# Kernel optimization log

Measured on AMD Instinct MI355X. Metric: run time of the kernel, lower is better.

## Reference

```python
import jax, jax.numpy as jnp
import numpy as np

B, Cin, Cout, H, W, K, S, P = 8, 128, 128, 64, 64, 3, 1, 1


def setup_inputs() -> dict:
    key = jax.random.key(0)
    k1, k2, k3 = jax.random.split(key, 3)
    x = jax.random.normal(k1, (B, Cin, H, W), jnp.float32)
    # offset-predicting conv weight (zero-init in the original; use small random for a nontrivial test)
    w_offset = jax.random.normal(k2, (2 * K * K, Cin, K, K), jnp.float32) * 0.01
    # deformable conv weight, uniform(-stdv, stdv) with stdv = 1/sqrt(Cin*K*K)
    stdv = 1.0 / np.sqrt(Cin * K * K)
    w = jax.random.uniform(k3, (Cout, Cin, K, K), jnp.float32, -stdv, stdv)
    return {"x": x, "w_offset": w_offset, "w": w}


def _conv2d(x, w, stride, pad):
    return jax.lax.conv_general_dilated(
        x, w, (stride, stride), [(pad, pad), (pad, pad)],
        dimension_numbers=("NCHW", "OIHW", "NCHW"))


def _deform_conv(x, offset, w, stride, pad):
    # x: [B,C,H,W]; offset: [B,2*K*K,Ho,Wo] as (dy,dx) pairs per kernel tap; w: [Cout,C,K,K]
    Bb, C, Hh, Ww = x.shape
    Co, _, Kk, _ = w.shape
    _, _, Ho, Wo = offset.shape
    KK = Kk * Kk
    off = offset.reshape(Bb, KK, 2, Ho, Wo)
    dy, dx = off[:, :, 0], off[:, :, 1]              # [B,KK,Ho,Wo]

    ky, kx = jnp.meshgrid(jnp.arange(Kk), jnp.arange(Kk), indexing="ij")
    ky = ky.reshape(KK).astype(x.dtype)
    kx = kx.reshape(KK).astype(x.dtype)
    oy = (jnp.arange(Ho) * stride - pad).astype(x.dtype)
    ox = (jnp.arange(Wo) * stride - pad).astype(x.dtype)

    # absolute sampling coordinates per kernel tap: [B,KK,Ho,Wo]
    py = oy[None, None, :, None] + ky[None, :, None, None] + dy
    px = ox[None, None, None, :] + kx[None, :, None, None] + dx

    y0 = jnp.floor(py)
    x0 = jnp.floor(px)
    ly = py - y0
    lx = px - x0
    y0i = y0.astype(jnp.int32)
    x0i = x0.astype(jnp.int32)

    xf = x.reshape(Bb, C, Hh * Ww)

    def gather(yi, xi):
        valid = (yi >= 0) & (yi < Hh) & (xi >= 0) & (xi < Ww)
        yc = jnp.clip(yi, 0, Hh - 1)
        xc = jnp.clip(xi, 0, Ww - 1)
        idx = (yc * Ww + xc).reshape(Bb, -1)          # [B, KK*Ho*Wo]
        v = jax.vmap(lambda xb, ib: xb[:, ib])(xf, idx)  # [B, C, KK*Ho*Wo]
        return v * valid.reshape(Bb, 1, -1).astype(x.dtype)

    v00 = gather(y0i, x0i)
    v01 = gather(y0i, x0i + 1)
    v10 = gather(y0i + 1, x0i)
    v11 = gather(y0i + 1, x0i + 1)

    wy = ly.reshape(Bb, 1, -1)
    wx = lx.reshape(Bb, 1, -1)
    sampled = (v00 * (1 - wy) * (1 - wx) + v01 * (1 - wy) * wx
               + v10 * wy * (1 - wx) + v11 * wy * wx)   # [B, C, KK*Ho*Wo]
    sampled = sampled.reshape(Bb, C, KK, Ho * Wo)

    out = jnp.einsum("bckl,ock->bol", sampled, w.reshape(Co, C, KK))
    return out.reshape(Bb, Co, Ho, Wo)


def reference(x, w_offset, w):
    offset = _conv2d(x, w_offset, S, P)   # [B, 2*K*K, Ho, Wo]
    return _deform_conv(x, offset, w, S, P)
```

## Files before the change

### kernel.cpp

```cpp
#include <hip/hip_runtime.h>
#include <hip/hip_bf16.h>
#include <math.h>


typedef _Float16 f16x8 __attribute__((ext_vector_type(8)));
typedef _Float16 h2    __attribute__((ext_vector_type(2)));
typedef float    f32x4 __attribute__((ext_vector_type(4)));

__global__ __launch_bounds__(256) void prep_weights(
    const float* __restrict__ w, const float* __restrict__ woff,
    _Float16* __restrict__ wT, _Float16* __restrict__ woffT) {
    int idx = blockIdx.x * 256 + threadIdx.x;
    if (idx < 147456) {
        int c  = idx & 127;
        int co = (idx >> 7) & 127;
        int kk = idx >> 14;
        wT[idx] = (_Float16)w[co * 1152 + c * 9 + kk];
    }
    if (idx < 36864) {
        int c  = idx & 127;
        int oc = (idx >> 7) & 31;
        int kk = idx >> 12;
        woffT[idx] = (oc < 18) ? (_Float16)woff[oc * 1152 + c * 9 + kk] : (_Float16)0.f;
    }
}

__global__ __launch_bounds__(256) void transpose_nchw_nhwc(
    const float* __restrict__ x, unsigned* __restrict__ xT) {
    __shared__ float tile[128][65];
    int bh = blockIdx.x;
    int b = bh >> 6, h = bh & 63;
    const float* src = x + b * 524288 + h * 64;
    for (int idx = threadIdx.x; idx < 8192; idx += 256) {
        int c = idx >> 6, ww = idx & 63;
        tile[c][ww] = src[c * 4096 + ww];
    }
    __syncthreads();
    unsigned* dst = xT + (size_t)bh * 4096;
    for (int idx = threadIdx.x; idx < 4096; idx += 256) {
        int ww = idx >> 6, c2 = (idx & 63) * 2;
        union { h2 h; unsigned u; } p;
        p.h = h2{(_Float16)tile[c2][ww], (_Float16)tile[c2 + 1][ww]};
        dst[idx] = p.u;
    }
}

__global__ __launch_bounds__(512, 4) void deform_fused(
    const _Float16* __restrict__ xT,
    const _Float16* __restrict__ wT,
    const _Float16* __restrict__ woffT,
    float* __restrict__ out) {
    __shared__ unsigned short s_tile[2][8192];
    __shared__ float  s_off[18][64];
    __shared__ int4   s_pix[576];
    __shared__ float4 s_wt[576];

    int raw = blockIdx.x;
    int b  = raw & 7;
    int ho = raw >> 3;
    int t = threadIdx.x, l = t & 63, w = t >> 6;
    int lr = l & 15, lg = l >> 4;
    const char* xb = (const char*)xT + (size_t)b * 1048576;

    {
        int m4 = w >> 1, n2 = w & 1;
        f16x8 A[2][4];
        f32x4 oacc = {0.f, 0.f, 0.f, 0.f};
        auto loadA = [&](int kk, f16x8* dst) {
            int y = ho + kk / 3 - 1;
            int xcol = m4 * 16 + lr + kk % 3 - 1;
            bool valid = ((unsigned)y < 64u) && ((unsigned)xcol < 64u);
            int yc = min(max(y, 0), 63), xc = min(max(xcol, 0), 63);
            const char* p = xb + ((yc * 64 + xc) * 128 + lg * 8) * 2;
            _Float16 m = (_Float16)(valid ? 1.f : 0.f);
#pragma unroll
            for (int kg = 0; kg < 4; ++kg)
                dst[kg] = *(const f16x8*)(p + kg * 64) * m;
        };
        loadA(0, A[0]);
#pragma unroll
        for (int kk = 0; kk < 9; ++kk) {
            if (kk < 8) loadA(kk + 1, A[(kk + 1) & 1]);
            const _Float16* wo = woffT + (kk * 32 + n2 * 16 + lr) * 128 + lg * 8;
#pragma unroll
            for (int kg = 0; kg < 4; ++kg)
                oacc = __builtin_amdgcn_mfma_f32_16x16x32_f16(
                    A[kk & 1][kg], *(const f16x8*)(wo + kg * 32), oacc, 0, 0, 0);
        }
        int oc = n2 * 16 + lr;
        if (oc < 18) {
#pragma unroll
            for (int r = 0; r < 4; ++r)
                s_off[oc][m4 * 16 + lg * 4 + r] = oacc[r];
        }
    }
    __syncthreads();

    for (int e = t; e < 576; e += 512) {
        int pos = e & 63, kk = e >> 6;
        float dy = s_off[2 * kk][pos], dx = s_off[2 * kk + 1][pos];
        float py = (float)(ho + kk / 3 - 1) + dy;
        float px = (float)(pos + kk % 3 - 1) + dx;
        float y0f = floorf(py), x0f = floorf(px);
        float ly = py - y0f, lx = px - x0f;
        int y0 = (int)y0f, x0 = (int)x0f;
        int y1 = y0 + 1, x1 = x0 + 1;
        float my0 = ((unsigned)y0 < 64u) ? 1.f : 0.f;
        float my1 = ((unsigned)y1 < 64u) ? 1.f : 0.f;
        float mx0 = ((unsigned)x0 < 64u) ? 1.f : 0.f;
        float mx1 = ((unsigned)x1 < 64u) ? 1.f : 0.f;
        int y0c = min(max(y0, 0), 63), y1c = min(max(y1, 0), 63);
        int x0c = min(max(x0, 0), 63), x1c = min(max(x1, 0), 63);
        s_pix[e] = make_int4((y0c * 64 + x0c) * 256, (y0c * 64 + x1c) * 256,
                             (y1c * 64 + x0c) * 256, (y1c * 64 + x1c) * 256);
        s_wt[e] = make_float4((1.f - ly) * (1.f - lx) * my0 * mx0,
                              (1.f - ly) * lx * my0 * mx1,
                              ly * (1.f - lx) * my1 * mx0,
                              ly * lx * my1 * mx1);
    }
    __syncthreads();

    int pg = t >> 5;
    int cq = t & 31;
    int cb = w * 16;
    int coff = cq * 8;
    f32x4 acc[4] = {{0.f,0.f,0.f,0.f},{0.f,0.f,0.f,0.f},{0.f,0.f,0.f,0.f},{0.f,0.f,0.f,0.f}};
    f16x8 W[2][4];
    uint2 u[4][4];

    auto issueW = [&](int kk, f16x8* Wd) {
        const _Float16* wr = wT + (kk * 128 + cb + lr) * 128 + lg * 8;
#pragma unroll
        for (int kg = 0; kg < 4; ++kg)
            Wd[kg] = *(const f16x8*)(wr + kg * 32);
    };
    auto issueG = [&](int kk) {
#pragma unroll
        for (int i = 0; i < 4; ++i) {
            int pos = pg + i * 16;
            int4 pix = s_pix[kk * 64 + pos];
            u[i][0] = *(const uint2*)(xb + pix.x + coff);
            u[i][1] = *(const uint2*)(xb + pix.y + coff);
            u[i][2] = *(const uint2*)(xb + pix.z + coff);
            u[i][3] = *(const uint2*)(xb + pix.w + coff);
        }
    };
    auto processW = [&](int kk, int buf) {
        char* tp = (char*)s_tile[buf];
#pragma unroll
        for (int i = 0; i < 4; ++i) {
            int pos = pg + i * 16;
            float4 wt = s_wt[kk * 64 + pos];
            h2 w0 = h2{(_Float16)wt.x, (_Float16)wt.x};
            h2 w1 = h2{(_Float16)wt.y, (_Float16)wt.y};
            h2 w2 = h2{(_Float16)wt.z, (_Float16)wt.z};
            h2 w3 = h2{(_Float16)wt.w, (_Float16)wt.w};
            union { uint2 u2; h2 h[2]; } a0, a1, a2, a3, r;
            a0.u2 = u[i][0]; a1.u2 = u[i][1]; a2.u2 = u[i][2]; a3.u2 = u[i][3];
            r.h[0] = w0 * a0.h[0] + w1 * a1.h[0] + w2 * a2.h[0] + w3 * a3.h[0];
            r.h[1] = w0 * a0.h[1] + w1 * a1.h[1] + w2 * a2.h[1] + w3 * a3.h[1];
            *(uint2*)(tp + pos * 256 + (((cq >> 1) ^ (pos & 7)) << 4) + (cq & 1) * 8) = r.u2;
        }
    };

    issueW(0, W[0]);
    issueG(0);
    processW(0, 0);
    __syncthreads();

#pragma unroll
    for (int kk = 0; kk < 9; ++kk) {
        if (kk < 8) {
            issueW(kk + 1, W[(kk + 1) & 1]);
            issueG(kk + 1);
        }
        __builtin_amdgcn_sched_barrier(0);
        {
            char* rp = (char*)s_tile[kk & 1];
#pragma unroll
            for (int kg = 0; kg < 4; ++kg) {
                int slot = kg * 4 + lg;
#pragma unroll
                for (int n = 0; n < 4; ++n) {
                    int row = n * 16 + lr;
                    f16x8 Bf = *(const f16x8*)(rp + row * 256 + ((slot ^ (row & 7)) << 4));
                    acc[n] = __builtin_amdgcn_mfma_f32_16x16x32_f16(W[kk & 1][kg], Bf, acc[n], 0, 0, 0);
                }
            }
        }
        __builtin_amdgcn_sched_barrier(0);
        if (kk < 8) processW(kk + 1, (kk + 1) & 1);
        __syncthreads();
    }

    float* ob = out + ((size_t)(b * 128 + cb + lg * 4)) * 4096 + ho * 64;
#pragma unroll
    for (int n = 0; n < 4; ++n) {
#pragma unroll
        for (int r = 0; r < 4; ++r)
            ob[r * 4096 + n * 16 + lr] = acc[n][r];
    }
}

extern "C" void kernel_launch(void* const* d_in, const int* in_sizes, int n_in,
                              void* d_out, int out_size, void* d_ws, size_t ws_size,
                              hipStream_t stream) {
    const float* x    = (const float*)d_in[0];
    const float* woff = (const float*)d_in[1];
    const float* w    = (const float*)d_in[2];
    float* out = (float*)d_out;

    _Float16* wT    = (_Float16*)d_ws;
    _Float16* woffT = (_Float16*)((char*)d_ws + 294912);
    _Float16* xT    = (_Float16*)((char*)d_ws + 368640);

    prep_weights<<<576, 256, 0, stream>>>(w, woff, wT, woffT);
    transpose_nchw_nhwc<<<512, 256, 0, stream>>>(x, (unsigned*)xT);
    deform_fused<<<512, 512, 0, stream>>>(xT, wT, woffT, out);
}
```

Before: 144.5 us.

## Split each output row across two blocks with half-width tiles and wider gathers

Each block now handles 32 output pixels of a row instead of 64, which doubles the grid to 1024 blocks and raises launch bounds to 8 waves per SIMD. Shared memory is roughly halved, and pixel indices are stored as ushort4. The gather now loads 16-byte chunks per thread, one pixel per 16 threads, instead of 8-byte chunks. The main weights are reloaded each tap without double buffering. The aim is higher occupancy and more latency hiding for the gather, at the cost of redundant offset-conv work: half the waves compute duplicate offsets, and every block reloads the full weight set.

```diff
diff --git a/kernel.cpp b/kernel.cpp
--- a/kernel.cpp
+++ b/kernel.cpp
@@ -45,62 +45,66 @@
     }
 }
 
-__global__ __launch_bounds__(512, 4) void deform_fused(
+__global__ __launch_bounds__(512, 8) void deform_fused(
     const _Float16* __restrict__ xT,
     const _Float16* __restrict__ wT,
     const _Float16* __restrict__ woffT,
     float* __restrict__ out) {
-    __shared__ unsigned short s_tile[2][8192];
-    __shared__ float  s_off[18][64];
-    __shared__ int4   s_pix[576];
-    __shared__ float4 s_wt[576];
+    __shared__ unsigned short s_tile[2][4096];
+    __shared__ ushort4 s_pix[288];
+    __shared__ float4  s_wt[288];
+    __shared__ float   s_off[18][32];
 
     int raw = blockIdx.x;
-    int b  = raw & 7;
-    int ho = raw >> 3;
+    int b    = raw & 7;
+    int rest = raw >> 3;
+    int ho   = rest >> 1;
+    int pos0 = (rest & 1) * 32;
     int t = threadIdx.x, l = t & 63, w = t >> 6;
     int lr = l & 15, lg = l >> 4;
     const char* xb = (const char*)xT + (size_t)b * 1048576;
 
     {
-        int m4 = w >> 1, n2 = w & 1;
-        f16x8 A[2][4];
+        int m = w & 1, n = (w >> 1) & 1, dup = w >> 2;
+        f16x8 A[2][4], Bc[4];
         f32x4 oacc = {0.f, 0.f, 0.f, 0.f};
         auto loadA = [&](int kk, f16x8* dst) {
-            int y = ho + kk / 3 - 1;
-            int xcol = m4 * 16 + lr + kk % 3 - 1;
-            bool valid = ((unsigned)y < 64u) && ((unsigned)xcol < 64u);
-            int yc = min(max(y, 0), 63), xc = min(max(xcol, 0), 63);
-            const char* p = xb + ((yc * 64 + xc) * 128 + lg * 8) * 2;
-            _Float16 m = (_Float16)(valid ? 1.f : 0.f);
+            int y  = ho + kk / 3 - 1;
+            int xc = pos0 + m * 16 + lr + kk % 3 - 1;
+            bool valid = ((unsigned)y < 64u) && ((unsigned)xc < 64u);
+            int yc = min(max(y, 0), 63), xcc = min(max(xc, 0), 63);
+            const char* p = xb + ((yc * 64 + xcc) << 8) + lg * 16;
+            _Float16 mk = (_Float16)(valid ? 1.f : 0.f);
 #pragma unroll
             for (int kg = 0; kg < 4; ++kg)
-                dst[kg] = *(const f16x8*)(p + kg * 64) * m;
+                dst[kg] = *(const f16x8*)(p + kg * 64) * mk;
         };
         loadA(0, A[0]);
 #pragma unroll
         for (int kk = 0; kk < 9; ++kk) {
+            const _Float16* wo = woffT + ((kk * 32 + n * 16 + lr) << 7) + lg * 8;
+#pragma unroll
+            for (int kg = 0; kg < 4; ++kg)
+                Bc[kg] = *(const f16x8*)(wo + kg * 32);
             if (kk < 8) loadA(kk + 1, A[(kk + 1) & 1]);
-            const _Float16* wo = woffT + (kk * 32 + n2 * 16 + lr) * 128 + lg * 8;
 #pragma unroll
             for (int kg = 0; kg < 4; ++kg)
-                oacc = __builtin_amdgcn_mfma_f32_16x16x32_f16(
-                    A[kk & 1][kg], *(const f16x8*)(wo + kg * 32), oacc, 0, 0, 0);
+                oacc = __builtin_amdgcn_mfma_f32_16x16x32_f16(A[kk & 1][kg], Bc[kg], oacc, 0, 0, 0);
         }
-        int oc = n2 * 16 + lr;
-        if (oc < 18) {
+        int oc = n * 16 + lr;
+        if (dup == 0 && oc < 18) {
 #pragma unroll
             for (int r = 0; r < 4; ++r)
-                s_off[oc][m4 * 16 + lg * 4 + r] = oacc[r];
+                s_off[oc][m * 16 + lg * 4 + r] = oacc[r];
         }
     }
     __syncthreads();
 
-    for (int e = t; e < 576; e += 512) {
-        int pos = e & 63, kk = e >> 6;
-        float dy = s_off[2 * kk][pos], dx = s_off[2 * kk + 1][pos];
+    if (t < 288) {
+        int p32 = t & 31, kk = t >> 5;
+        float dy = s_off[2 * kk][p32], dx = s_off[2 * kk + 1][p32];
         float py = (float)(ho + kk / 3 - 1) + dy;
-        float px = (float)(pos + kk % 3 - 1) + dx;
+        float px = (float)(pos0 + p32 + kk % 3 - 1) + dx;
         float y0f = floorf(py), x0f = floorf(px);
         float ly = py - y0f, lx = px - x0f;
         int y0 = (int)y0f, x0 = (int)x0f;
@@ -111,69 +115,59 @@
         float mx1 = ((unsigned)x1 < 64u) ? 1.f : 0.f;
         int y0c = min(max(y0, 0), 63), y1c = min(max(y1, 0), 63);
         int x0c = min(max(x0, 0), 63), x1c = min(max(x1, 0), 63);
-        s_pix[e] = make_int4((y0c * 64 + x0c) * 256, (y0c * 64 + x1c) * 256,
-                             (y1c * 64 + x0c) * 256, (y1c * 64 + x1c) * 256);
-        s_wt[e] = make_float4((1.f - ly) * (1.f - lx) * my0 * mx0,
+        s_pix[t] = make_ushort4((unsigned short)(y0c * 64 + x0c),
+                                (unsigned short)(y0c * 64 + x1c),
+                                (unsigned short)(y1c * 64 + x0c),
+                                (unsigned short)(y1c * 64 + x1c));
+        s_wt[t] = make_float4((1.f - ly) * (1.f - lx) * my0 * mx0,
                               (1.f - ly) * lx * my0 * mx1,
                               ly * (1.f - lx) * my1 * mx0,
                               ly * lx * my1 * mx1);
     }
     __syncthreads();
 
-    int pg = t >> 5;
-    int cq = t & 31;
-    int cb = w * 16;
-    int coff = cq * 8;
-    f32x4 acc[4] = {{0.f,0.f,0.f,0.f},{0.f,0.f,0.f,0.f},{0.f,0.f,0.f,0.f},{0.f,0.f,0.f,0.f}};
-    f16x8 W[2][4];
-    uint2 u[4][4];
-
-    auto issueW = [&](int kk, f16x8* Wd) {
-        const _Float16* wr = wT + (kk * 128 + cb + lr) * 128 + lg * 8;
+    int p32 = t >> 4;
+    int cq  = t & 15;
+    int cb  = w * 16;
+    f32x4 acc[2] = {{0.f,0.f,0.f,0.f},{0.f,0.f,0.f,0.f}};
+    uint4 u[4];
+
+    auto issueG = [&](int kk) {
+        ushort4 pc = s_pix[kk * 32 + p32];
+        const char* bb = xb + cq * 16;
+        u[0] = *(const uint4*)(bb + ((int)pc.x << 8));
+        u[1] = *(const uint4*)(bb + ((int)pc.y << 8));
+        u[2] = *(const uint4*)(bb + ((int)pc.z << 8));
+        u[3] = *(const uint4*)(bb + ((int)pc.w << 8));
+    };
+    auto blend = [&](int kk, int buf) {
+        float4 wt = s_wt[kk * 32 + p32];
+        h2 w0 = h2{(_Float16)wt.x, (_Float16)wt.x};
+        h2 w1 = h2{(_Float16)wt.y, (_Float16)wt.y};
+        h2 w2 = h2{(_Float16)wt.z, (_Float16)wt.z};
+        h2 w3 = h2{(_Float16)wt.w, (_Float16)wt.w};
+        union { uint4 q; h2 h[4]; } c0, c1, c2, c3, r;
+        c0.q = u[0]; c1.q = u[1]; c2.q = u[2]; c3.q = u[3];
+#pragma unroll
+        for (int j = 0; j < 4; ++j)
+            r.h[j] = w0 * c0.h[j] + w1 * c1.h[j] + w2 * c2.h[j] + w3 * c3.h[j];
+        char* tpb = (char*)s_tile[buf];
+        *(uint4*)(tpb + p32 * 256 + ((cq ^ (p32 & 15)) << 4)) = r.q;
+    };
+
+    issueG(0);
+    blend(0, 0);
+    __syncthreads();
+
+#pragma unroll
+    for (int kk = 0; kk < 9; ++kk) {
+        f16x8 Wf[4];
+        const _Float16* wr = wT + ((kk * 128 + cb + lr) << 7) + lg * 8;
 #pragma unroll
         for (int kg = 0; kg < 4; ++kg)
-            Wd[kg] = *(const f16x8*)(wr + kg * 32);
-    };
-    auto issueG = [&](int kk) {
-#pragma unroll
-        for (int i = 0; i < 4; ++i) {
-            int pos = pg + i * 16;
-            int4 pix = s_pix[kk * 64 + pos];
-            u[i][0] = *(const uint2*)(xb + pix.x + coff);
-            u[i][1] = *(const uint2*)(xb + pix.y + coff);
-            u[i][2] = *(const uint2*)(xb + pix.z + coff);
-            u[i][3] = *(const uint2*)(xb + pix.w + coff);
-        }
-    };
-    auto processW = [&](int kk, int buf) {
-        char* tp = (char*)s_tile[buf];
-#pragma unroll
-        for (int i = 0; i < 4; ++i) {
-            int pos = pg + i * 16;
-            float4 wt = s_wt[kk * 64 + pos];
-            h2 w0 = h2{(_Float16)wt.x, (_Float16)wt.x};
-            h2 w1 = h2{(_Float16)wt.y, (_Float16)wt.y};
-            h2 w2 = h2{(_Float16)wt.z, (_Float16)wt.z};
-            h2 w3 = h2{(_Float16)wt.w, (_Float16)wt.w};
-            union { uint2 u2; h2 h[2]; } a0, a1, a2, a3, r;
-            a0.u2 = u[i][0]; a1.u2 = u[i][1]; a2.u2 = u[i][2]; a3.u2 = u[i][3];
-            r.h[0] = w0 * a0.h[0] + w1 * a1.h[0] + w2 * a2.h[0] + w3 * a3.h[0];
-            r.h[1] = w0 * a0.h[1] + w1 * a1.h[1] + w2 * a2.h[1] + w3 * a3.h[1];
-            *(uint2*)(tp + pos * 256 + (((cq >> 1) ^ (pos & 7)) << 4) + (cq & 1) * 8) = r.u2;
-        }
-    };
-
-    issueW(0, W[0]);
-    issueG(0);
-    processW(0, 0);
-    __syncthreads();
-
-#pragma unroll
-    for (int kk = 0; kk < 9; ++kk) {
-        if (kk < 8) {
-            issueW(kk + 1, W[(kk + 1) & 1]);
-            issueG(kk + 1);
-        }
+            Wf[kg] = *(const f16x8*)(wr + kg * 32);
+        __builtin_amdgcn_sched_barrier(0);
+        if (kk < 8) issueG(kk + 1);
         __builtin_amdgcn_sched_barrier(0);
         {
             char* rp = (char*)s_tile[kk & 1];
@@ -181,21 +175,21 @@
             for (int kg = 0; kg < 4; ++kg) {
                 int slot = kg * 4 + lg;
 #pragma unroll
-                for (int n = 0; n < 4; ++n) {
+                for (int n = 0; n < 2; ++n) {
                     int row = n * 16 + lr;
-                    f16x8 Bf = *(const f16x8*)(rp + row * 256 + ((slot ^ (row & 7)) << 4));
-                    acc[n] = __builtin_amdgcn_mfma_f32_16x16x32_f16(W[kk & 1][kg], Bf, acc[n], 0, 0, 0);
+                    f16x8 Bf = *(const f16x8*)(rp + row * 256 + ((slot ^ (row & 15)) << 4));
+                    acc[n] = __builtin_amdgcn_mfma_f32_16x16x32_f16(Wf[kg], Bf, acc[n], 0, 0, 0);
                 }
             }
         }
         __builtin_amdgcn_sched_barrier(0);
-        if (kk < 8) processW(kk + 1, (kk + 1) & 1);
+        if (kk < 8) blend(kk + 1, (kk + 1) & 1);
         __syncthreads();
     }
 
-    float* ob = out + ((size_t)(b * 128 + cb + lg * 4)) * 4096 + ho * 64;
-#pragma unroll
-    for (int n = 0; n < 4; ++n) {
+    float* ob = out + ((size_t)(b * 128 + cb + lg * 4)) * 4096 + ho * 64 + pos0;
+#pragma unroll
+    for (int n = 0; n < 2; ++n) {
 #pragma unroll
         for (int r = 0; r < 4; ++r)
             ob[r * 4096 + n * 16 + lr] = acc[n][r];
@@ -216,5 +210,5 @@
 
     prep_weights<<<576, 256, 0, stream>>>(w, woff, wT, woffT);
     transpose_nchw_nhwc<<<512, 256, 0, stream>>>(x, (unsigned*)xT);
-    deform_fused<<<512, 512, 0, stream>>>(xT, wT, woffT, out);
-}
+    deform_fused<<<1024, 512, 0, stream>>>(xT, wT, woffT, out);
+}
```

Result: slower. 183.5 us (+27.0%).
